# Kernel optimization log

Measured on AMD Instinct MI355X. Metric: run time of the kernel, lower is better.

Reference implementation:

```python
import jax, jax.numpy as jnp
import numpy as np

N = 50000      # node_size
D = 256        # node_F == rel_F (ent_F)
R = 1000       # rel_size
E = 300000     # triple_size == n_edges
DEPTH = 2
KSEL = E // 2  # rows rewritten by W_orth transform
NPROXY = 128


def l2n(x):
    # tf.nn.l2_normalize with eps=1e-12
    return x * jax.lax.rsqrt(jnp.maximum(jnp.sum(x * x, axis=-1, keepdims=True), 1e-12))


def setup_inputs() -> dict:
    key = jax.random.key(0)
    ks = jax.random.split(key, 12)
    features = jax.random.normal(ks[0], (N, D), jnp.float32)
    rel_emb = jax.random.normal(ks[1], (R, D), jnp.float32)
    p = jax.random.normal(ks[2], (N, 1), jnp.float32)            # dynamic_node_kernel
    w_keys = jax.random.normal(ks[3], (DEPTH, D, D), jnp.float32) / np.float32(np.sqrt(D))
    attn_kernels = jax.random.normal(ks[4], (DEPTH, D, 1), jnp.float32) * 0.1
    proxy = jax.random.normal(ks[5], (NPROXY, D * (DEPTH + 1)), jnp.float32) * 0.05
    gate_kernel = jax.random.normal(ks[6], (D * (DEPTH + 1), D * (DEPTH + 1)), jnp.float32) / np.float32(np.sqrt(D * (DEPTH + 1)))
    adj_row = jnp.sort(jax.random.randint(ks[7], (E,), 0, N))    # destination (segment) ids, sorted
    adj_col = jax.random.randint(ks[8], (E,), 0, N)              # neighbor ids
    rel_ids = jax.random.randint(ks[9], (E,), 0, R)              # relation id per triple/edge
    rel_vals = jax.random.uniform(ks[10], (E,), jnp.float32)     # sparse_val per triple
    new_indices = jax.random.randint(ks[11], (KSEL,), 0, E)      # rows updated by w_key
    return dict(features=features, rel_emb=rel_emb, p=p, w_keys=w_keys,
                attn_kernels=attn_kernels, proxy=proxy, gate_kernel=gate_kernel,
                rel_vals=rel_vals, adj_row=adj_row, adj_col=adj_col,
                rel_ids=rel_ids, new_indices=new_indices)


def reference(features, rel_emb, p, w_keys, attn_kernels, proxy, gate_kernel,
              rel_vals, adj_row, adj_col, rel_ids, new_indices):
    tanh_p = jnp.tanh(p)                                   # [N,1]
    feats = features * tanh_p                              # use_p scaling (activation=None -> identity)
    outputs = [feats]
    for l in range(DEPTH):
        # sparse (triple,rel) x rel_emb : one relation per triple -> gather + scale
        rels_sum = rel_vals[:, None] * rel_emb[rel_ids]    # [E,D]
        rels_sum = l2n(rels_sum)
        # W_orth: transform a subset of rows by w_key, scatter back
        src = rels_sum[new_indices] @ w_keys[l]            # [KSEL,D]
        rels_sum = rels_sum.at[new_indices].set(src)
        neighs = feats[adj_col]                            # [E,D] gather
        rels_sum = rels_sum * tanh_p[adj_col]              # use_p on neighbors
        # Householder-style reflection of neighbor features
        neighs = neighs - 2.0 * jnp.sum(neighs * rels_sum, axis=1, keepdims=True) * rels_sum
        # per-edge attention logits, softmax over incoming edges of each row node
        att = (rels_sum @ attn_kernels[l])[:, 0]           # [E]
        m = jax.ops.segment_max(att, adj_row, num_segments=N)      # [N]
        att = jnp.exp(att - m[adj_row])
        s = jax.ops.segment_sum(att, adj_row, num_segments=N)      # [N]
        att = att / s[adj_row]
        # weighted scatter-aggregate
        feats = jax.ops.segment_sum(neighs * att[:, None], adj_row, num_segments=N)  # [N,D]
        feats = feats * tanh_p
        outputs.append(feats)
    out = jnp.concatenate(outputs, axis=-1)                # [N, D*(DEPTH+1)]
    proxy_att = jax.nn.softmax(l2n(out) @ l2n(proxy).T, axis=-1)   # [N,128]
    proxy_feature = out - proxy_att @ proxy
    gate = jax.nn.sigmoid(proxy_feature @ gate_kernel)
    out = gate * out + (1.0 - gate) * proxy_feature
    return (out, p)
```

## Files before the change

kernel.cpp:

```cpp
#include <hip/hip_runtime.h>
#include <math.h>

#define D 256
#define DCAT 768
#define NPX 128
#define QSTR 896
#define CSTR 136

typedef __attribute__((ext_vector_type(8))) short bf16x8;
typedef __attribute__((ext_vector_type(4))) float f32x4;

__device__ __forceinline__ short cvt_bf16(float f){
  union { float f; unsigned u; } v; v.f = f;
  unsigned r = v.u + 0x7FFF + ((v.u >> 16) & 1);
  return (short)(r >> 16);
}
__device__ __forceinline__ float bf2f(short s){
  union { float f; unsigned u; } v; v.u = ((unsigned)(unsigned short)s) << 16;
  return v.f;
}

__device__ __forceinline__ float waveSum(float v){
#pragma unroll
  for(int o=32;o>=1;o>>=1) v += __shfl_xor(v,o,64);
  return v;
}
__device__ __forceinline__ float waveMax(float v){
#pragma unroll
  for(int o=32;o>=1;o>>=1) v = fmaxf(v,__shfl_xor(v,o,64));
  return v;
}

__global__ void k_setup(const float* __restrict__ rel_emb, const float* __restrict__ attn,
                        const float* __restrict__ w_keys, const float* __restrict__ proxy,
                        const float* __restrict__ gatek, const float* __restrict__ p,
                        const int* __restrict__ adj_row, const int* __restrict__ new_idx,
                        float* __restrict__ ss_rel, float* __restrict__ att_n,
                        float* __restrict__ att_t, short* __restrict__ reb,
                        short* __restrict__ rwb, short* __restrict__ pn,
                        short* __restrict__ proxyb, short* __restrict__ BG,
                        short* __restrict__ Bt2, float* __restrict__ tp,
                        int* __restrict__ rs, unsigned char* __restrict__ flag,
                        float* __restrict__ pout, int R_, int n, int e, int ksel){
  __shared__ float tile[32][33];
  __shared__ float sm[4];
  const int b = blockIdx.x, tid = threadIdx.x;
  const int lane = tid & 63, wv = tid >> 6;

  if(b < R_){
    int r = b, d = tid;
    float v = rel_emb[(size_t)r*D+d];
    reb[(size_t)r*D+d] = cvt_bf16(v);
    float s = waveSum(v*v);
    if(lane==0) sm[wv]=s;
    __syncthreads();
    if(tid==0) ss_rel[r]=sm[0]+sm[1]+sm[2]+sm[3];
    __syncthreads();
    for(int l=0;l<2;l++){
      float dd = waveSum(v*attn[l*D+d]);
      if(lane==0) sm[wv]=dd;
      __syncthreads();
      if(tid==0) att_n[(size_t)l*R_+r]=sm[0]+sm[1]+sm[2]+sm[3];
      __syncthreads();
    }
  } else if(b < 3*R_){
    int l = (b-R_) / R_, r = (b-R_) % R_, d = tid;
    const float* W = w_keys + (size_t)l*D*D;
    const float* ak = attn + (size_t)l*D;
    const float* row = rel_emb + (size_t)r*D;
    float acc=0.f;
#pragma unroll 4
    for(int k=0;k<D;k++) acc = fmaf(row[k], W[(size_t)k*D+d], acc);
    rwb[(size_t)l*R_*D + (size_t)r*D + d]=cvt_bf16(acc);
    float dd = waveSum(acc*ak[d]);
    if(lane==0) sm[wv]=dd;
    __syncthreads();
    if(tid==0) att_t[(size_t)l*R_+r]=sm[0]+sm[1]+sm[2]+sm[3];
  } else if(b < 3*R_+128){
    int j = b - 3*R_;
    float v0 = proxy[(size_t)j*DCAT + tid];
    float v1 = proxy[(size_t)j*DCAT + 256 + tid];
    float v2 = proxy[(size_t)j*DCAT + 512 + tid];
    proxyb[(size_t)j*DCAT + tid]       = cvt_bf16(v0);
    proxyb[(size_t)j*DCAT + 256 + tid] = cvt_bf16(v1);
    proxyb[(size_t)j*DCAT + 512 + tid] = cvt_bf16(v2);
    float ssum = waveSum(v0*v0 + v1*v1 + v2*v2);
    if(lane==0) sm[wv]=ssum;
    __syncthreads();
    float scale = rsqrtf(fmaxf(sm[0]+sm[1]+sm[2]+sm[3],1e-12f));
    pn[(size_t)j*DCAT + tid]       = cvt_bf16(v0*scale);
    pn[(size_t)j*DCAT + 256 + tid] = cvt_bf16(v1*scale);
    pn[(size_t)j*DCAT + 512 + tid] = cvt_bf16(v2*scale);
  } else if(b < 3*R_+128+576+96){
    const float* in; short* out; int R, C, ldo, t;
    if(b < 3*R_+128+576){ t = b-(3*R_+128);     in=gatek; out=BG;  R=DCAT; C=DCAT; ldo=QSTR; }
    else                { t = b-(3*R_+128+576); in=proxy; out=Bt2; R=NPX;  C=DCAT; ldo=NPX;  }
    int bx = (t%24)*32, by = (t/24)*32;
    int tx = tid & 31, ty = tid >> 5;
    for(int i=ty;i<32;i+=8){
      int rr = by+i, cc = bx+tx;
      if(rr<R && cc<C) tile[i][tx] = in[(size_t)rr*C + cc];
    }
    __syncthreads();
    for(int i=ty;i<32;i+=8){
      int cc = bx+i, rr = by+tx;
      if(cc<C && rr<R) out[(size_t)cc*ldo + rr] = cvt_bf16(tile[tx][i]);
    }
  } else {
    int t = b - (3*R_+128+576+96);
    int i = t*256 + tid;
    if(i<n){ float pv = p[i]; tp[i]=tanhf(pv); pout[i]=pv; }
    if(i<=n){
      int lo=0, hi=e;
      while(lo<hi){ int mid=(lo+hi)>>1; if(adj_row[mid]<i) lo=mid+1; else hi=mid; }
      rs[i]=lo;
    }
    if(i<ksel) flag[new_idx[i]] = 1;
  }
}

__global__ void k_tcast(const float* __restrict__ in, short* __restrict__ out,
                        int R, int C, int ldo, int coff, float sign){
  __shared__ float tile[32][33];
  int bx = blockIdx.x*32, by = blockIdx.y*32;
  for(int i=threadIdx.y;i<32;i+=8){
    int rr = by+i, cc = bx+threadIdx.x;
    if(rr<R && cc<C) tile[i][threadIdx.x] = in[(size_t)rr*C + cc];
  }
  __syncthreads();
  for(int i=threadIdx.y;i<32;i+=8){
    int cc = bx+i, rr = by+threadIdx.x;
    if(cc<C && rr<R) out[(size_t)cc*ldo + coff + rr] = cvt_bf16(sign*tile[threadIdx.x][i]);
  }
}

__global__ void k_init0(const float* __restrict__ features, const float* __restrict__ tp,
                        short* __restrict__ Q, float* __restrict__ ssn, int n){
  __shared__ float sm[4];
  int row = blockIdx.x, d = threadIdx.x;
  float v = features[(size_t)row*D + d] * tp[row];
  Q[(size_t)row*QSTR + d] = cvt_bf16(v);
  int lane=d&63, wid=d>>6;
  float s = waveSum(v*v);
  if(lane==0) sm[wid]=s;
  __syncthreads();
  if(d==0) ssn[row] = sm[0]+sm[1]+sm[2]+sm[3];
}

__global__ void k_agg(const int* __restrict__ rs, const int* __restrict__ adj_col,
                      const int* __restrict__ rel_ids, const float* __restrict__ rel_vals,
                      const unsigned char* __restrict__ flag, const float* __restrict__ tp,
                      const float* __restrict__ ss_rel, const float* __restrict__ att_n,
                      const float* __restrict__ att_t, const short* __restrict__ reb,
                      const short* __restrict__ rwb, short* __restrict__ Q,
                      float* __restrict__ ssn, int n, int layer){
  int wid = threadIdx.x>>6, lane = threadIdx.x&63;
  int node = blockIdx.x*4 + wid;
  if(node>=n) return;
  int s = rs[node], e = rs[node+1];
  float accq[16];
#pragma unroll
  for(int k=0;k<16;k++) accq[k]=0.f;

  auto logit = [&](int i)->float{
    int rid = rel_ids[i]; float rv = rel_vals[i];
    float a = 0.f;
    if(rv>0.f){
      float t = tp[adj_col[i]];
      float sc = rv*rsqrtf(fmaxf(rv*rv*ss_rel[rid],1e-12f));
      a = t*sc*(flag[i]? att_t[rid] : att_n[rid]);
    }
    return a;
  };

  if(e > s){
    float aF = 0.f, mxl = -INFINITY;
    {
      int i = s + lane;
      if(i < e){
        aF = logit(i);
        mxl = aF;
        for(i += 64; i < e; i += 64) mxl = fmaxf(mxl, logit(i));
      }
    }
    float mx = waveMax(mxl);
    float sel = (s+lane < e) ? __expf(aF - mx) : 0.f;
    for(int i = s+64+lane; i < e; i += 64) sel += __expf(logit(i) - mx);
    float se = waveSum(sel);
    float inv = 1.f/se;

    int qid = lane>>4, ql = lane&15;
    int j0 = s + qid;
    bool valid = j0 < e;
    int col=0, rid=0; float rv=0.f; bool fl=false;
    bf16x8 pn0={}, pn1={}, pr0={}, pr1={};
    if(valid){
      col=adj_col[j0]; rid=rel_ids[j0]; rv=rel_vals[j0]; fl=flag[j0];
      const short* np = Q + (size_t)col*QSTR + layer*D + ql*16;
      pn0 = *(const bf16x8*)np; pn1 = *(const bf16x8*)(np+8);
      if(rv>0.f){
        const short* rp = (fl? rwb : reb) + (size_t)rid*D + ql*16;
        pr0 = *(const bf16x8*)rp; pr1 = *(const bf16x8*)(rp+8);
      }
    }
    for(int i0=s; i0<e; i0+=4){
      int jn = i0 + 4 + qid;
      bool vn = jn < e;
      int coln=0, ridn=0; float rvn=0.f; bool fln=false;
      bf16x8 qn0={}, qn1={}, qr0={}, qr1={};
      if(vn){
        coln=adj_col[jn]; ridn=rel_ids[jn]; rvn=rel_vals[jn]; fln=flag[jn];
        const short* np = Q + (size_t)coln*QSTR + layer*D + ql*16;
        qn0 = *(const bf16x8*)np; qn1 = *(const bf16x8*)(np+8);
        if(rvn>0.f){
          const short* rp = (fln? rwb : reb) + (size_t)ridn*D + ql*16;
          qr0 = *(const bf16x8*)rp; qr1 = *(const bf16x8*)(rp+8);
        }
      }
      float w=0.f, coef=0.f;
      float nbv[16], rbv[16];
#pragma unroll
      for(int k=0;k<8;k++){
        nbv[k]=bf2f(pn0[k]); nbv[k+8]=bf2f(pn1[k]);
        rbv[k]=bf2f(pr0[k]); rbv[k+8]=bf2f(pr1[k]);
      }
      if(valid){
        if(rv>0.f){
          float t = tp[col];
          float sc = rv*rsqrtf(fmaxf(rv*rv*ss_rel[rid],1e-12f));
          float dp = 0.f;
#pragma unroll
          for(int k=0;k<16;k++) dp += nbv[k]*rbv[k];
#pragma unroll
          for(int o=1;o<16;o<<=1) dp += __shfl_xor(dp,o,64);
          float a = t*sc*(fl? att_t[rid] : att_n[rid]);
          w = __expf(a-mx)*inv;
          coef = 2.f*t*t*sc*sc*dp;
        } else {
          w = __expf(-mx)*inv;
        }
      }
#pragma unroll
      for(int k=0;k<16;k++) accq[k] += w*(nbv[k] - coef*rbv[k]);

      valid=vn; col=coln; rid=ridn; rv=rvn; fl=fln;
      pn0=qn0; pn1=qn1; pr0=qr0; pr1=qr1;
    }
  }
#pragma unroll
  for(int k=0;k<16;k++){
    float v = accq[k];
    v += __shfl_xor(v,16,64);
    v += __shfl_xor(v,32,64);
    accq[k] = v;
  }
  if(lane < 16){
    float t0 = tp[node];
    bf16x8 o0, o1;
    float pss = 0.f;
#pragma unroll
    for(int k=0;k<8;k++){
      o0[k]=cvt_bf16(accq[k]*t0); o1[k]=cvt_bf16(accq[k+8]*t0);
      pss += accq[k]*accq[k] + accq[k+8]*accq[k+8];
    }
    short* op = Q + (size_t)node*QSTR + (layer+1)*D + lane*16;
    *(bf16x8*)op = o0;
    *(bf16x8*)(op+8) = o1;
#pragma unroll
    for(int o=1;o<16;o<<=1) pss += __shfl_xor(pss,o,64);
    if(lane==0) ssn[node] += pss * t0 * t0;
  }
}

template<int LDA_, int LDB_, int NTOT, int KC>
__global__ __launch_bounds__(256,2) void k_gemm(
    const short* __restrict__ A, const short* __restrict__ Bt,
    float* __restrict__ outF, int M)
{
  __shared__ short smem[3][2][128*32];
  const int tid = threadIdx.x;
  const int lane = tid & 63, w = tid >> 6;
  const int wm = w >> 1, wn = w & 1;
  const int bn = blockIdx.x * 128, bm = blockIdx.y * 128;

  const short* Ag = A  + (size_t)bm * LDA_;
  const short* Bg = Bt + (size_t)bn * LDB_;

  auto stage = [&](int buf, int k0){
#pragma unroll
    for(int c=0;c<2;++c){
      int u = c*256 + tid;
      int row = u >> 2;
      int cb = ((u & 3) ^ ((u >> 3) & 3)) * 8;
      __builtin_amdgcn_global_load_lds(
        (const __attribute__((address_space(1))) unsigned int*)(Ag + (size_t)row*LDA_ + k0 + cb),
        (__attribute__((address_space(3))) unsigned int*)&smem[buf][0][u*8], 16, 0, 0);
      __builtin_amdgcn_global_load_lds(
        (const __attribute__((address_space(1))) unsigned int*)(Bg + (size_t)row*LDB_ + k0 + cb),
        (__attribute__((address_space(3))) unsigned int*)&smem[buf][1][u*8], 16, 0, 0);
    }
  };

  f32x4 acc[4][4] = {};
  const int lr = lane & 15, kg = lane >> 4;
  const int ksw = (kg ^ ((lr >> 1) & 3)) * 8;
  constexpr int NT = KC / 32;

  stage(0, 0);
  stage(1, 32);
  for(int t=0; t<NT; ++t){
    if(t+1 < NT) asm volatile("s_waitcnt vmcnt(4)" ::: "memory");
    else         asm volatile("s_waitcnt vmcnt(0)" ::: "memory");
    __builtin_amdgcn_s_barrier();
    __builtin_amdgcn_sched_barrier(0);
    const short* Al = &smem[t%3][0][0];
    const short* Bl = &smem[t%3][1][0];
    bf16x8 af[4], bfr[4];
#pragma unroll
    for(int i=0;i<4;++i) af[i] = *(const bf16x8*)(Al + (wm*64 + i*16 + lr)*32 + ksw);
#pragma unroll
    for(int j=0;j<4;++j) bfr[j] = *(const bf16x8*)(Bl + (wn*64 + j*16 + lr)*32 + ksw);
    if(t+2 < NT) stage((t+2)%3, (t+2)*32);
    __builtin_amdgcn_s_setprio(1);
#pragma unroll
    for(int i=0;i<4;++i)
#pragma unroll
      for(int j=0;j<4;++j)
        acc[i][j] = __builtin_amdgcn_mfma_f32_16x16x32_bf16(af[i], bfr[j], acc[i][j], 0, 0, 0);
    __builtin_amdgcn_s_setprio(0);
  }

  const int row0 = bm + wm*64 + (lane>>4)*4;
  const int col0 = bn + wn*64 + lr;
#pragma unroll
  for(int i=0;i<4;++i)
#pragma unroll
    for(int j=0;j<4;++j)
#pragma unroll
      for(int r=0;r<4;++r){
        int row = row0 + i*16 + r;
        if(row < M) outF[(size_t)row*NTOT + col0 + j*16] = acc[i][j][r];
      }
}

__global__ __launch_bounds__(256,2) void k_pr(
    short* __restrict__ Q, const short* __restrict__ pn,
    const float* __restrict__ ssn, int M)
{
  __shared__ short smem[3][2][128*32];
  const int tid = threadIdx.x, lane = tid & 63, w = tid >> 6;
  const int wm = w >> 1, wn = w & 1;
  int nwg = gridDim.y;
  int orig = blockIdx.y;
  int q = nwg>>3, rm = nwg&7, xcd = orig&7, lid = orig>>3;
  int wg = (xcd<rm ? xcd*(q+1) : rm*(q+1)+(xcd-rm)*q) + lid;
  const int bm = wg*128;

  const short* Ag = Q + (size_t)bm * QSTR;
  const short* Bg = pn;

  auto stage = [&](int buf, int k0){
#pragma unroll
    for(int c=0;c<2;++c){
      int u = c*256 + tid;
      int row = u >> 2;
      int cb = ((u & 3) ^ ((u >> 3) & 3)) * 8;
      __builtin_amdgcn_global_load_lds(
        (const __attribute__((address_space(1))) unsigned int*)(Ag + (size_t)row*QSTR + k0 + cb),
        (__attribute__((address_space(3))) unsigned int*)&smem[buf][0][u*8], 16, 0, 0);
      __builtin_amdgcn_global_load_lds(
        (const __attribute__((address_space(1))) unsigned int*)(Bg + (size_t)row*DCAT + k0 + cb),
        (__attribute__((address_space(3))) unsigned int*)&smem[buf][1][u*8], 16, 0, 0);
    }
  };

  f32x4 acc[4][4] = {};
  const int lr = lane & 15, kg = lane >> 4;
  const int ksw = (kg ^ ((lr >> 1) & 3)) * 8;
  constexpr int NT = DCAT / 32;

  stage(0, 0);
  stage(1, 32);
  for(int t=0; t<NT; ++t){
    if(t+1 < NT) asm volatile("s_waitcnt vmcnt(4)" ::: "memory");
    else         asm volatile("s_waitcnt vmcnt(0)" ::: "memory");
    __builtin_amdgcn_s_barrier();
    __builtin_amdgcn_sched_barrier(0);
    const short* Al = &smem[t%3][0][0];
    const short* Bl = &smem[t%3][1][0];
    bf16x8 af[4], bfr[4];
#pragma unroll
    for(int i=0;i<4;++i) af[i] = *(const bf16x8*)(Al + (wm*64 + i*16 + lr)*32 + ksw);
#pragma unroll
    for(int j=0;j<4;++j) bfr[j] = *(const bf16x8*)(Bl + (wn*64 + j*16 + lr)*32 + ksw);
    if(t+2 < NT) stage((t+2)%3, (t+2)*32);
    __builtin_amdgcn_s_setprio(1);
#pragma unroll
    for(int i=0;i<4;++i)
#pragma unroll
      for(int j=0;j<4;++j)
        acc[i][j] = __builtin_amdgcn_mfma_f32_16x16x32_bf16(af[i], bfr[j], acc[i][j], 0, 0, 0);
    __builtin_amdgcn_s_setprio(0);
  }

  __syncthreads();
  short* lg = (short*)smem;
  const int row0l = wm*64 + kg*4;
  const int col0l = wn*64 + lr;
#pragma unroll
  for(int i=0;i<4;++i){
#pragma unroll
    for(int j=0;j<4;++j){
#pragma unroll
      for(int r=0;r<4;++r){
        int rl = row0l + i*16 + r;
        int rg = bm + rl;
        float s = (rg < M) ? rsqrtf(fmaxf(ssn[rg],1e-12f)) : 0.f;
        lg[rl*132 + col0l + j*16] = cvt_bf16(acc[i][j][r] * s);
      }
    }
  }
  __syncthreads();
  for(int k2=0;k2<32;++k2){
    int rl = w*32 + k2;
    float a = bf2f(lg[rl*132 + lane]);
    float b = bf2f(lg[rl*132 + 64 + lane]);
    float m = waveMax(fmaxf(a,b));
    float ea = __expf(a-m), eb = __expf(b-m);
    float sm_ = waveSum(ea+eb);
    float inv = 1.f/sm_;
    size_t rg = (size_t)(bm + rl);
    Q[rg*QSTR + DCAT + lane]      = cvt_bf16(ea*inv);
    Q[rg*QSTR + DCAT + 64 + lane] = cvt_bf16(eb*inv);
  }
}

__global__ __launch_bounds__(256,2) void k_go(
    short* __restrict__ Q, const short* __restrict__ BG,
    const short* __restrict__ Bt2, float* __restrict__ outF, int M)
{
  __shared__ short smem[3][2][128*32];
  const int tid = threadIdx.x, lane = tid & 63, w = tid >> 6;
  const int wm = w >> 1, wn = w & 1;
  const int gx = gridDim.x;
  int nwg = gx*gridDim.y;
  int orig = blockIdx.y*gx + blockIdx.x;
  int q = nwg>>3, rm = nwg&7, xcd = orig&7, lid = orig>>3;
  int wg = (xcd<rm ? xcd*(q+1) : rm*(q+1)+(xcd-rm)*q) + lid;
  const int bn = (wg%gx)*128, bm = (wg/gx)*128;
  const int lr = lane & 15, kg = lane >> 4;

  const short* Ag = Q  + (size_t)bm * QSTR;
  const short* Bg = BG + (size_t)bn * QSTR;

  auto stage = [&](int buf, int k0){
#pragma unroll
    for(int c=0;c<2;++c){
      int u = c*256 + tid;
      int row = u >> 2;
      int cb = ((u & 3) ^ ((u >> 3) & 3)) * 8;
      __builtin_amdgcn_global_load_lds(
        (const __attribute__((address_space(1))) unsigned int*)(Ag + (size_t)row*QSTR + k0 + cb),
        (__attribute__((address_space(3))) unsigned int*)&smem[buf][0][u*8], 16, 0, 0);
      __builtin_amdgcn_global_load_lds(
        (const __attribute__((address_space(1))) unsigned int*)(Bg + (size_t)row*QSTR + k0 + cb),
        (__attribute__((address_space(3))) unsigned int*)&smem[buf][1][u*8], 16, 0, 0);
    }
  };

  stage(0, 0);
  stage(1, 32);

  f32x4 acc[4][4] = {};
#pragma unroll
  for(int ks=0; ks<4; ++ks){
    bf16x8 af[4], bb[4];
#pragma unroll
    for(int i=0;i<4;++i)
      af[i] = *(const bf16x8*)(Q + (size_t)(bm + wm*64 + i*16 + lr)*QSTR + DCAT + ks*32 + kg*8);
#pragma unroll
    for(int j=0;j<4;++j)
      bb[j] = *(const bf16x8*)(Bt2 + (size_t)(bn + wn*64 + j*16 + lr)*NPX + ks*32 + kg*8);
#pragma unroll
    for(int i=0;i<4;++i)
#pragma unroll
      for(int j=0;j<4;++j)
        acc[i][j] = __builtin_amdgcn_mfma_f32_16x16x32_bf16(af[i], bb[j], acc[i][j], 0, 0, 0);
  }
  short4 pvb[4][4];
#pragma unroll
  for(int i=0;i<4;++i)
#pragma unroll
    for(int j=0;j<4;++j){
      pvb[i][j].x = cvt_bf16(acc[i][j][0]);
      pvb[i][j].y = cvt_bf16(acc[i][j][1]);
      pvb[i][j].z = cvt_bf16(acc[i][j][2]);
      pvb[i][j].w = cvt_bf16(acc[i][j][3]);
      acc[i][j] = (f32x4){0.f,0.f,0.f,0.f};
    }

  const int ksw = (kg ^ ((lr >> 1) & 3)) * 8;
  constexpr int NT = QSTR / 32;
  for(int t=0; t<NT; ++t){
    if(t+1 < NT) asm volatile("s_waitcnt vmcnt(4)" ::: "memory");
    else         asm volatile("s_waitcnt vmcnt(0)" ::: "memory");
    __builtin_amdgcn_s_barrier();
    __builtin_amdgcn_sched_barrier(0);
    const short* Al = &smem[t%3][0][0];
    const short* Bl = &smem[t%3][1][0];
    bf16x8 af[4], bfr[4];
#pragma unroll
    for(int i=0;i<4;++i) af[i] = *(const bf16x8*)(Al + (wm*64 + i*16 + lr)*32 + ksw);
#pragma unroll
    for(int j=0;j<4;++j) bfr[j] = *(const bf16x8*)(Bl + (wn*64 + j*16 + lr)*32 + ksw);
    if(t+2 < NT) stage((t+2)%3, (t+2)*32);
    __builtin_amdgcn_s_setprio(1);
#pragma unroll
    for(int i=0;i<4;++i)
#pragma unroll
      for(int j=0;j<4;++j)
        acc[i][j] = __builtin_amdgcn_mfma_f32_16x16x32_bf16(af[i], bfr[j], acc[i][j], 0, 0, 0);
    __builtin_amdgcn_s_setprio(0);
  }

  __syncthreads();
  short* cst = (short*)smem;
  const int row0l = wm*64 + kg*4;
  const int col0l = wn*64 + lr;
#pragma unroll
  for(int i=0;i<4;++i){
#pragma unroll
    for(int j=0;j<4;++j){
      float pv4[4] = { bf2f(pvb[i][j].x), bf2f(pvb[i][j].y), bf2f(pvb[i][j].z), bf2f(pvb[i][j].w) };
#pragma unroll
      for(int r2=0;r2<4;++r2){
        float g = 1.f/(1.f+__expf(-acc[i][j][r2]));
        cst[(row0l + i*16 + r2)*CSTR + col0l + j*16] = cvt_bf16((1.f-g)*pv4[r2]);
      }
    }
  }
  __syncthreads();
  const int rl0 = tid>>4, c0 = (tid&15)*8;
#pragma unroll
  for(int rr=0; rr<8; ++rr){
    int rl = rl0 + rr*16;
    int rg = bm + rl;
    if(rg >= M) continue;
    bf16x8 c8  = *(const bf16x8*)(cst + rl*CSTR + c0);
    bf16x8 oc8 = *(const bf16x8*)(Q + (size_t)rg*QSTR + bn + c0);
    float ov[8];
#pragma unroll
    for(int k=0;k<8;k++) ov[k] = bf2f(oc8[k]) - bf2f(c8[k]);
    *(float4*)(outF + (size_t)rg*DCAT + bn + c0)     = make_float4(ov[0],ov[1],ov[2],ov[3]);
    *(float4*)(outF + (size_t)rg*DCAT + bn + c0 + 4) = make_float4(ov[4],ov[5],ov[6],ov[7]);
  }
}

extern "C" void kernel_launch(void* const* d_in, const int* in_sizes, int n_in,
                              void* d_out, int out_size, void* d_ws, size_t ws_size,
                              hipStream_t stream){
  const float* features = (const float*)d_in[0];
  const float* rel_emb  = (const float*)d_in[1];
  const float* p        = (const float*)d_in[2];
  const float* w_keys   = (const float*)d_in[3];
  const float* attn     = (const float*)d_in[4];
  const float* proxy    = (const float*)d_in[5];
  const float* gatek    = (const float*)d_in[6];
  const float* rel_vals = (const float*)d_in[7];
  const int* adj_row    = (const int*)d_in[8];
  const int* adj_col    = (const int*)d_in[9];
  const int* rel_ids    = (const int*)d_in[10];
  const int* new_idx    = (const int*)d_in[11];

  const int n    = in_sizes[2];
  const int r    = in_sizes[1]/D;
  const int e    = in_sizes[7];
  const int ksel = in_sizes[11];
  const size_t Mpad = ((size_t)n + 127) & ~(size_t)127;

  char* ws = (char*)d_ws;
  size_t off=0;
  auto alloc=[&](size_t bytes)->void*{ void* pp = ws+off; off=(off+bytes+255)&~(size_t)255; return pp; };
  float* tp      = (float*)alloc((size_t)n*4);
  int*   rs      = (int*)alloc((size_t)(n+1)*4);
  unsigned char* flag = (unsigned char*)alloc((size_t)e);
  float* ss_rel  = (float*)alloc((size_t)r*4);
  float* att_n   = (float*)alloc((size_t)2*r*4);
  float* att_t   = (float*)alloc((size_t)2*r*4);
  short* reb     = (short*)alloc((size_t)r*D*2);
  short* rwb     = (short*)alloc((size_t)2*r*D*2);
  short* pn      = (short*)alloc((size_t)NPX*DCAT*2);
  short* proxyb  = (short*)alloc((size_t)NPX*DCAT*2);
  short* Bt2     = (short*)alloc((size_t)DCAT*NPX*2);
  short* BG      = (short*)alloc((size_t)DCAT*QSTR*2);
  float* MxF     = (float*)alloc((size_t)NPX*DCAT*4);
  float* ssn     = (float*)alloc(Mpad*4);
  short* Q       = (short*)alloc(Mpad*QSTR*2);

  float* outF = (float*)d_out;
  float* pout = (float*)d_out + (size_t)n*DCAT;

  hipMemsetAsync(flag, 0, (size_t)e, stream);
  hipMemsetAsync(Q + (size_t)n*QSTR, 0, (Mpad-(size_t)n)*QSTR*2, stream);

  {
    int prep_n = (ksel > n+1 ? ksel : n+1);
    int nprep = (prep_n+255)/256;
    int nblocks = 3*r + 128 + 576 + 96 + nprep;
    k_setup<<<nblocks,256,0,stream>>>(rel_emb, attn, w_keys, proxy, gatek, p,
                                      adj_row, new_idx,
                                      ss_rel, att_n, att_t, reb, rwb, pn, proxyb,
                                      BG, Bt2, tp, rs, flag, pout, r, n, e, ksel);
  }
  k_gemm<DCAT, QSTR, DCAT, DCAT><<<dim3(DCAT/128,1),256,0,stream>>>(proxyb, BG, MxF, NPX);
  k_tcast<<<dim3(DCAT/32, NPX/32), dim3(32,8), 0, stream>>>(MxF, BG, NPX, DCAT, QSTR, DCAT, -1.f);

  k_init0<<<n,256,0,stream>>>(features,tp,Q,ssn,n);
  for(int l=0;l<2;l++)
    k_agg<<<(n+3)/4,256,0,stream>>>(rs,adj_col,rel_ids,rel_vals,flag,tp,ss_rel,
                                    att_n+(size_t)l*r, att_t+(size_t)l*r, reb,
                                    rwb+(size_t)l*r*D, Q, ssn, n, l);

  int mt = (int)(Mpad/128);
  k_pr<<<dim3(1, mt),256,0,stream>>>(Q, pn, ssn, n);
  k_go<<<dim3(DCAT/128, mt),256,0,stream>>>(Q, BG, Bt2, outF, n);
}
```

Baseline: 434.2 us.

## Fold proxy×gate GEMM and feature init into the setup kernel

Removes three separate launches: the small MFMA GEMM for proxy@gate_kernel, its transpose-cast kernel, and the per-row feature init kernel. The proxy×gate product now runs as an fp32 tiled SIMT matmul inside k_setup and is written negated and transposed straight into BG. The feature scaling and bf16 cast into Q are also handled by extra k_setup blocks, which recompute tanh(p) locally. This cuts launch overhead and intermediate buffers, at the cost of a much larger setup grid and slower scalar FMA math for the GEMM blocks.

```diff
diff --git a/kernel.cpp b/kernel.cpp
--- a/kernel.cpp
+++ b/kernel.cpp
@@ -34,18 +34,23 @@
 __global__ void k_setup(const float* __restrict__ rel_emb, const float* __restrict__ attn,
                         const float* __restrict__ w_keys, const float* __restrict__ proxy,
                         const float* __restrict__ gatek, const float* __restrict__ p,
+                        const float* __restrict__ features,
                         const int* __restrict__ adj_row, const int* __restrict__ new_idx,
                         float* __restrict__ ss_rel, float* __restrict__ att_n,
                         float* __restrict__ att_t, short* __restrict__ reb,
                         short* __restrict__ rwb, short* __restrict__ pn,
-                        short* __restrict__ proxyb, short* __restrict__ BG,
-                        short* __restrict__ Bt2, float* __restrict__ tp,
-                        int* __restrict__ rs, unsigned char* __restrict__ flag,
-                        float* __restrict__ pout, int R_, int n, int e, int ksel){
+                        short* __restrict__ BG, short* __restrict__ Bt2,
+                        float* __restrict__ tp, int* __restrict__ rs,
+                        unsigned char* __restrict__ flag, float* __restrict__ pout,
+                        short* __restrict__ Q, float* __restrict__ ssn,
+                        int R_, int n, int e, int ksel, int nprep){
   __shared__ float tile[32][33];
+  __shared__ float tile2[32][33];
   __shared__ float sm[4];
   const int b = blockIdx.x, tid = threadIdx.x;
   const int lane = tid & 63, wv = tid >> 6;
+  const int B2 = 3*R_+128, B3 = B2+576, B4 = B3+96, B5 = B4+96;
+  const int B6 = B5+nprep;
 
   if(b < R_){
     int r = b, d = tid;
@@ -76,14 +81,11 @@
     if(lane==0) sm[wv]=dd;
     __syncthreads();
     if(tid==0) att_t[(size_t)l*R_+r]=sm[0]+sm[1]+sm[2]+sm[3];
-  } else if(b < 3*R_+128){
+  } else if(b < B2){
     int j = b - 3*R_;
     float v0 = proxy[(size_t)j*DCAT + tid];
     float v1 = proxy[(size_t)j*DCAT + 256 + tid];
     float v2 = proxy[(size_t)j*DCAT + 512 + tid];
-    proxyb[(size_t)j*DCAT + tid]       = cvt_bf16(v0);
-    proxyb[(size_t)j*DCAT + 256 + tid] = cvt_bf16(v1);
-    proxyb[(size_t)j*DCAT + 512 + tid] = cvt_bf16(v2);
     float ssum = waveSum(v0*v0 + v1*v1 + v2*v2);
     if(lane==0) sm[wv]=ssum;
     __syncthreads();
@@ -91,10 +93,10 @@
     pn[(size_t)j*DCAT + tid]       = cvt_bf16(v0*scale);
     pn[(size_t)j*DCAT + 256 + tid] = cvt_bf16(v1*scale);
     pn[(size_t)j*DCAT + 512 + tid] = cvt_bf16(v2*scale);
-  } else if(b < 3*R_+128+576+96){
+  } else if(b < B4){
     const float* in; short* out; int R, C, ldo, t;
-    if(b < 3*R_+128+576){ t = b-(3*R_+128);     in=gatek; out=BG;  R=DCAT; C=DCAT; ldo=QSTR; }
-    else                { t = b-(3*R_+128+576); in=proxy; out=Bt2; R=NPX;  C=DCAT; ldo=NPX;  }
+    if(b < B3){ t = b-B2; in=gatek; out=BG;  R=DCAT; C=DCAT; ldo=QSTR; }
+    else      { t = b-B3; in=proxy; out=Bt2; R=NPX;  C=DCAT; ldo=NPX;  }
     int bx = (t%24)*32, by = (t/24)*32;
     int tx = tid & 31, ty = tid >> 5;
     for(int i=ty;i<32;i+=8){
@@ -106,8 +108,33 @@
       int cc = bx+i, rr = by+tx;
       if(cc<C && rr<R) out[(size_t)cc*ldo + rr] = cvt_bf16(tile[tx][i]);
     }
-  } else {
-    int t = b - (3*R_+128+576+96);
+  } else if(b < B5){
+    int t = b - B4;
+    int it = t / 24, jt = t % 24;
+    int i0 = it*32, j0 = jt*32;
+    int tx = tid & 31, ty = tid >> 5;
+    float acc4[4] = {0.f,0.f,0.f,0.f};
+    for(int k0=0;k0<DCAT;k0+=32){
+      for(int rr=ty;rr<32;rr+=8){
+        tile[rr][tx]  = proxy[(size_t)(i0+rr)*DCAT + k0+tx];
+        tile2[rr][tx] = gatek[(size_t)(k0+rr)*DCAT + j0+tx];
+      }
+      __syncthreads();
+#pragma unroll 8
+      for(int kk=0;kk<32;kk++){
+        float bv = tile2[kk][tx];
+        acc4[0] = fmaf(tile[ty][kk],    bv, acc4[0]);
+        acc4[1] = fmaf(tile[ty+8][kk],  bv, acc4[1]);
+        acc4[2] = fmaf(tile[ty+16][kk], bv, acc4[2]);
+        acc4[3] = fmaf(tile[ty+24][kk], bv, acc4[3]);
+      }
+      __syncthreads();
+    }
+#pragma unroll
+    for(int k=0;k<4;k++)
+      BG[(size_t)(j0+tx)*QSTR + DCAT + i0 + ty + 8*k] = cvt_bf16(-acc4[k]);
+  } else if(b < B6){
+    int t = b - B5;
     int i = t*256 + tid;
     if(i<n){ float pv = p[i]; tp[i]=tanhf(pv); pout[i]=pv; }
     if(i<=n){
@@ -116,35 +143,18 @@
       rs[i]=lo;
     }
     if(i<ksel) flag[new_idx[i]] = 1;
-  }
-}
-
-__global__ void k_tcast(const float* __restrict__ in, short* __restrict__ out,
-                        int R, int C, int ldo, int coff, float sign){
-  __shared__ float tile[32][33];
-  int bx = blockIdx.x*32, by = blockIdx.y*32;
-  for(int i=threadIdx.y;i<32;i+=8){
-    int rr = by+i, cc = bx+threadIdx.x;
-    if(rr<R && cc<C) tile[i][threadIdx.x] = in[(size_t)rr*C + cc];
-  }
-  __syncthreads();
-  for(int i=threadIdx.y;i<32;i+=8){
-    int cc = bx+i, rr = by+threadIdx.x;
-    if(cc<C && rr<R) out[(size_t)cc*ldo + coff + rr] = cvt_bf16(sign*tile[threadIdx.x][i]);
-  }
-}
-
-__global__ void k_init0(const float* __restrict__ features, const float* __restrict__ tp,
-                        short* __restrict__ Q, float* __restrict__ ssn, int n){
-  __shared__ float sm[4];
-  int row = blockIdx.x, d = threadIdx.x;
-  float v = features[(size_t)row*D + d] * tp[row];
-  Q[(size_t)row*QSTR + d] = cvt_bf16(v);
-  int lane=d&63, wid=d>>6;
-  float s = waveSum(v*v);
-  if(lane==0) sm[wid]=s;
-  __syncthreads();
-  if(d==0) ssn[row] = sm[0]+sm[1]+sm[2]+sm[3];
+  } else {
+    int row = b - B6;
+    if(row < n){
+      float t0 = tanhf(p[row]);
+      float v = features[(size_t)row*D + tid] * t0;
+      Q[(size_t)row*QSTR + tid] = cvt_bf16(v);
+      float s = waveSum(v*v);
+      if(lane==0) sm[wv]=s;
+      __syncthreads();
+      if(tid==0) ssn[row] = sm[0]+sm[1]+sm[2]+sm[3];
+    }
+  }
 }
 
 __global__ void k_agg(const int* __restrict__ rs, const int* __restrict__ adj_col,
@@ -270,77 +280,6 @@
     for(int o=1;o<16;o<<=1) pss += __shfl_xor(pss,o,64);
     if(lane==0) ssn[node] += pss * t0 * t0;
   }
-}
-
-template<int LDA_, int LDB_, int NTOT, int KC>
-__global__ __launch_bounds__(256,2) void k_gemm(
-    const short* __restrict__ A, const short* __restrict__ Bt,
-    float* __restrict__ outF, int M)
-{
-  __shared__ short smem[3][2][128*32];
-  const int tid = threadIdx.x;
-  const int lane = tid & 63, w = tid >> 6;
-  const int wm = w >> 1, wn = w & 1;
-  const int bn = blockIdx.x * 128, bm = blockIdx.y * 128;
-
-  const short* Ag = A  + (size_t)bm * LDA_;
-  const short* Bg = Bt + (size_t)bn * LDB_;
-
-  auto stage = [&](int buf, int k0){
-#pragma unroll
-    for(int c=0;c<2;++c){
-      int u = c*256 + tid;
-      int row = u >> 2;
-      int cb = ((u & 3) ^ ((u >> 3) & 3)) * 8;
-      __builtin_amdgcn_global_load_lds(
-        (const __attribute__((address_space(1))) unsigned int*)(Ag + (size_t)row*LDA_ + k0 + cb),
-        (__attribute__((address_space(3))) unsigned int*)&smem[buf][0][u*8], 16, 0, 0);
-      __builtin_amdgcn_global_load_lds(
-        (const __attribute__((address_space(1))) unsigned int*)(Bg + (size_t)row*LDB_ + k0 + cb),
-        (__attribute__((address_space(3))) unsigned int*)&smem[buf][1][u*8], 16, 0, 0);
-    }
-  };
-
-  f32x4 acc[4][4] = {};
-  const int lr = lane & 15, kg = lane >> 4;
-  const int ksw = (kg ^ ((lr >> 1) & 3)) * 8;
-  constexpr int NT = KC / 32;
-
-  stage(0, 0);
-  stage(1, 32);
-  for(int t=0; t<NT; ++t){
-    if(t+1 < NT) asm volatile("s_waitcnt vmcnt(4)" ::: "memory");
-    else         asm volatile("s_waitcnt vmcnt(0)" ::: "memory");
-    __builtin_amdgcn_s_barrier();
-    __builtin_amdgcn_sched_barrier(0);
-    const short* Al = &smem[t%3][0][0];
-    const short* Bl = &smem[t%3][1][0];
-    bf16x8 af[4], bfr[4];
-#pragma unroll
-    for(int i=0;i<4;++i) af[i] = *(const bf16x8*)(Al + (wm*64 + i*16 + lr)*32 + ksw);
-#pragma unroll
-    for(int j=0;j<4;++j) bfr[j] = *(const bf16x8*)(Bl + (wn*64 + j*16 + lr)*32 + ksw);
-    if(t+2 < NT) stage((t+2)%3, (t+2)*32);
-    __builtin_amdgcn_s_setprio(1);
-#pragma unroll
-    for(int i=0;i<4;++i)
-#pragma unroll
-      for(int j=0;j<4;++j)
-        acc[i][j] = __builtin_amdgcn_mfma_f32_16x16x32_bf16(af[i], bfr[j], acc[i][j], 0, 0, 0);
-    __builtin_amdgcn_s_setprio(0);
-  }
-
-  const int row0 = bm + wm*64 + (lane>>4)*4;
-  const int col0 = bn + wn*64 + lr;
-#pragma unroll
-  for(int i=0;i<4;++i)
-#pragma unroll
-    for(int j=0;j<4;++j)
-#pragma unroll
-      for(int r=0;r<4;++r){
-        int row = row0 + i*16 + r;
-        if(row < M) outF[(size_t)row*NTOT + col0 + j*16] = acc[i][j][r];
-      }
 }
 
 __global__ __launch_bounds__(256,2) void k_pr(
@@ -590,10 +529,8 @@
   short* reb     = (short*)alloc((size_t)r*D*2);
   short* rwb     = (short*)alloc((size_t)2*r*D*2);
   short* pn      = (short*)alloc((size_t)NPX*DCAT*2);
-  short* proxyb  = (short*)alloc((size_t)NPX*DCAT*2);
   short* Bt2     = (short*)alloc((size_t)DCAT*NPX*2);
   short* BG      = (short*)alloc((size_t)DCAT*QSTR*2);
-  float* MxF     = (float*)alloc((size_t)NPX*DCAT*4);
   float* ssn     = (float*)alloc(Mpad*4);
   short* Q       = (short*)alloc(Mpad*QSTR*2);
 
@@ -606,16 +543,14 @@
   {
     int prep_n = (ksel > n+1 ? ksel : n+1);
     int nprep = (prep_n+255)/256;
-    int nblocks = 3*r + 128 + 576 + 96 + nprep;
-    k_setup<<<nblocks,256,0,stream>>>(rel_emb, attn, w_keys, proxy, gatek, p,
+    int nblocks = 3*r + 128 + 576 + 96 + 96 + nprep + n;
+    k_setup<<<nblocks,256,0,stream>>>(rel_emb, attn, w_keys, proxy, gatek, p, features,
                                       adj_row, new_idx,
-                                      ss_rel, att_n, att_t, reb, rwb, pn, proxyb,
-                                      BG, Bt2, tp, rs, flag, pout, r, n, e, ksel);
-  }
-  k_gemm<DCAT, QSTR, DCAT, DCAT><<<dim3(DCAT/128,1),256,0,stream>>>(proxyb, BG, MxF, NPX);
-  k_tcast<<<dim3(DCAT/32, NPX/32), dim3(32,8), 0, stream>>>(MxF, BG, NPX, DCAT, QSTR, DCAT, -1.f);
-
-  k_init0<<<n,256,0,stream>>>(features,tp,Q,ssn,n);
+                                      ss_rel, att_n, att_t, reb, rwb, pn,
+                                      BG, Bt2, tp, rs, flag, pout, Q, ssn,
+                                      r, n, e, ksel, nprep);
+  }
+
   for(int l=0;l<2;l++)
     k_agg<<<(n+3)/4,256,0,stream>>>(rs,adj_col,rel_ids,rel_vals,flag,tp,ss_rel,
                                     att_n+(size_t)l*r, att_t+(size_t)l*r, reb,
```

Result: no change. 436.8 us (median of 2 runs) (+0.6%).
